# Kernel tuning notes

Measured on AMD Instinct MI355X. Metric: run time of the kernel, lower is better.

## Reference

```python
import math
import jax, jax.numpy as jnp
import numpy as np

L, H = 4, 8  # num_layers, num_heads
SPARSE_FACTOR = 0.1
NEG = -1e9


def _ln(x, g, b, eps=1e-5):
    m = jnp.mean(x, axis=-1, keepdims=True)
    v = jnp.mean(jnp.square(x - m), axis=-1, keepdims=True)
    return (x - m) * jax.lax.rsqrt(v + eps) * g + b


def _pos_enc(S, D):
    # sinusoidal PE, shape (S, 1, D) matching pe.unsqueeze(0).transpose(0,1)[:S]
    pos = np.arange(S, dtype=np.float32)[:, None]
    div = np.exp(np.arange(0, D, 2, dtype=np.float32) * (-math.log(10000.0) / D))
    pe = np.zeros((S, D), dtype=np.float32)
    pe[:, 0::2] = np.sin(pos * div)
    pe[:, 1::2] = np.cos(pos * div)
    return jnp.asarray(pe)[:, None, :]


def setup_inputs() -> dict:
    key = jax.random.key(0)
    B, S, I, D, F = 128, 512, 64, 512, 2048
    ks = jax.random.split(key, 10)
    w = lambda k, shape: jax.random.normal(k, shape, jnp.float32) * 0.02
    return {
        'x': jax.random.normal(ks[0], (B, S, I), jnp.float32),
        'W_in': w(ks[1], (I, D)), 'b_in': jnp.zeros((D,), jnp.float32),
        'ln1_g': jnp.ones((L, D), jnp.float32), 'ln1_b': jnp.zeros((L, D), jnp.float32),
        'Wq': w(ks[2], (L, D, D)), 'Wk': w(ks[3], (L, D, D)), 'Wv': w(ks[4], (L, D, D)),
        'Wo': w(ks[5], (L, D, D)), 'bo': jnp.zeros((L, D), jnp.float32),
        'ln2_g': jnp.ones((L, D), jnp.float32), 'ln2_b': jnp.zeros((L, D), jnp.float32),
        'W1': w(ks[6], (L, D, F)), 'b1': jnp.zeros((L, F), jnp.float32),
        'W2': w(ks[7], (L, F, D)), 'b2': jnp.zeros((L, D), jnp.float32),
        'lnf_g': jnp.ones((D,), jnp.float32), 'lnf_b': jnp.zeros((D,), jnp.float32),
    }


def reference(x, W_in, b_in, ln1_g, ln1_b, Wq, Wk, Wv, Wo, bo,
              ln2_g, ln2_b, W1, b1, W2, b2, lnf_g, lnf_b):
    B, S, _ = x.shape
    D = W_in.shape[1]
    dk = D // H
    # source: scores last dim == batch (view+transpose quirk); k = max(1, int(B*0.1))
    topk = max(1, int(B * SPARSE_FACTOR))
    h = jnp.swapaxes(x, 0, 1) @ W_in + b_in          # (S,B,D)
    h = h * math.sqrt(D) + _pos_enc(S, D)

    def heads(z, w):
        return jnp.swapaxes((z @ w).reshape(S, B, H, dk), 1, 2)  # (S,H,B,dk)

    def body(h, p):
        g1, bb1, wq, wk, wv, wo, bo_, g2, bb2, w1, b1_, w2, b2_ = p
        y = _ln(h, g1, bb1)
        q, k, v = heads(y, wq), heads(y, wk), heads(y, wv)
        scores = jnp.einsum('shbd,shcd->shbc', q, k) / math.sqrt(dk)  # (S,H,B,B)
        kth = jax.lax.top_k(scores, topk)[0][..., -1:]
        scores = jnp.where(scores >= kth, scores, NEG)  # top-k sparsification
        attn = jax.nn.softmax(scores, axis=-1)
        ctx = jnp.einsum('shbc,shcd->shbd', attn, v)
        ctx = jnp.swapaxes(ctx, 1, 2).reshape(S, B, D)
        h = ctx @ wo + bo_ + h                       # attn out + residual
        f = jax.nn.gelu(_ln(h, g2, bb2) @ w1 + b1_, approximate=False) @ w2 + b2_
        return h + f, None

    h, _ = jax.lax.scan(body, h, (ln1_g, ln1_b, Wq, Wk, Wv, Wo, bo,
                                  ln2_g, ln2_b, W1, b1, W2, b2))
    h = _ln(h, lnf_g, lnf_b)
    return jnp.swapaxes(h, 0, 1)                     # (B,S,D)
```

## Files before the change

### kernel.cpp

```cpp
#include <hip/hip_runtime.h>
#include <math.h>

#define S_ 512
#define B_ 128
#define D_ 512
#define I_ 64
#define F_ 2048
#define H_ 8
#define DK_ 64
#define L_ 4
#define SB_ (S_*B_)

typedef unsigned short u16;
typedef unsigned int u32;
typedef __attribute__((ext_vector_type(4))) unsigned int u32x4;
typedef __attribute__((ext_vector_type(4))) float f32x4;

__device__ __forceinline__ u16 f2bf(float f){
  u32 x = __builtin_bit_cast(u32, f);
  x += 0x7fffu + ((x >> 16) & 1u);
  return (u16)(x >> 16);
}

__device__ __forceinline__ void mfma16(f32x4& c, const u32x4& a, const u32x4& b){
  asm volatile("v_mfma_f32_16x16x32_bf16 %0, %1, %2, %0" : "+v"(c) : "v"(a), "v"(b));
}

__device__ __forceinline__ void gload16(const u16* g, u16* l){
  __builtin_amdgcn_global_load_lds((const __attribute__((address_space(1))) unsigned int*)g,
                                   (__attribute__((address_space(3))) unsigned int*)l, 16, 0, 0);
}

__device__ __forceinline__ float gelu_fast(float x){
  float u = 0.7978845608028654f * fmaf(0.044715f*x*x, x, x);
  float ae = __expf(-2.f*fabsf(u));
  float th = (1.f - ae) / (1.f + ae);
  th = (u < 0.f) ? -th : th;
  return 0.5f * x * (1.f + th);
}

__global__ void pe_kernel(float* __restrict__ pe){
  int s = blockIdx.x, d = threadIdx.x;
  float e = expf((float)(d & ~1) * (-9.210340371976184f / (float)D_));
  float arg = (float)s * e;
  pe[s*D_ + d] = (d & 1) ? cosf(arg) : sinf(arg);
}

__global__ void transpose_bf16(const float* __restrict__ src, u16* __restrict__ dst,
                               int R, int C, size_t zstride){
  __shared__ float t[32][33];
  size_t sbase = (size_t)blockIdx.z * R * C;
  size_t dbase = (size_t)blockIdx.z * zstride;
  int r0 = blockIdx.y*32, c0 = blockIdx.x*32;
  int tx = threadIdx.x, ty = threadIdx.y;
  #pragma unroll
  for (int j=0;j<4;j++)
    t[ty+j*8][tx] = src[sbase + (size_t)(r0+ty+j*8)*C + c0+tx];
  __syncthreads();
  #pragma unroll
  for (int j=0;j<4;j++)
    dst[dbase + (size_t)(c0+ty+j*8)*R + r0+tx] = f2bf(t[tx][ty+j*8]);
}

__global__ __launch_bounds__(512) void inproj_kernel(const float* __restrict__ x,
    const float* __restrict__ Win, const float* __restrict__ bin,
    const float* __restrict__ pe, float* __restrict__ h){
  __shared__ float xs[8][64];
  int t = threadIdx.x;
  float w[64];
  #pragma unroll
  for (int i=0;i<64;i++) w[i] = Win[i*D_ + t];
  float bd = bin[t];
  int r0 = blockIdx.x * 128;
  for (int batch=0; batch<16; batch++){
    int rb = r0 + batch*8;
    {
      int rr = t >> 6, i = t & 63;
      int r = rb + rr;
      int s = r >> 7, b = r & 127;
      xs[rr][i] = x[((size_t)b*S_ + s)*I_ + i];
    }
    __syncthreads();
    float acc[8];
    #pragma unroll
    for (int rr=0;rr<8;rr++) acc[rr] = 0.f;
    #pragma unroll
    for (int i4=0;i4<16;i4++){
      f32x4 xv[8];
      #pragma unroll
      for (int rr=0;rr<8;rr++) xv[rr] = *(const f32x4*)&xs[rr][i4*4];
      #pragma unroll
      for (int rr=0;rr<8;rr++){
        acc[rr] = fmaf(xv[rr][0], w[i4*4+0], acc[rr]);
        acc[rr] = fmaf(xv[rr][1], w[i4*4+1], acc[rr]);
        acc[rr] = fmaf(xv[rr][2], w[i4*4+2], acc[rr]);
        acc[rr] = fmaf(xv[rr][3], w[i4*4+3], acc[rr]);
      }
    }
    #pragma unroll
    for (int rr=0;rr<8;rr++){
      int r = rb + rr;
      int s = r >> 7;
      h[(size_t)r*D_ + t] = (acc[rr] + bd) * 22.627416997969522f + pe[s*D_ + t];
    }
    __syncthreads();
  }
}

template<int FINAL>
__global__ __launch_bounds__(256) void ln_kernel(const float* __restrict__ hsrc,
    const float* __restrict__ g, const float* __restrict__ bb,
    u16* __restrict__ outb, float* __restrict__ outf){
  int row = blockIdx.x*4 + (threadIdx.x>>6);
  int lane = threadIdx.x & 63;
  const float* hr = hsrc + (size_t)row*D_ + lane*8;
  f32x4 a0 = *(const f32x4*)hr;
  f32x4 a1 = *(const f32x4*)(hr+4);
  float v[8];
  #pragma unroll
  for (int j=0;j<4;j++){ v[j]=a0[j]; v[4+j]=a1[j]; }
  float sum = 0.f;
  #pragma unroll
  for (int j=0;j<8;j++) sum += v[j];
  #pragma unroll
  for (int m=1;m<64;m<<=1) sum += __shfl_xor(sum, m);
  float mean = sum * (1.f/(float)D_);
  float s2 = 0.f;
  #pragma unroll
  for (int j=0;j<8;j++){ float dd = v[j]-mean; s2 = fmaf(dd,dd,s2); }
  #pragma unroll
  for (int m=1;m<64;m<<=1) s2 += __shfl_xor(s2, m);
  float inv = rsqrtf(s2*(1.f/(float)D_) + 1e-5f);
  f32x4 g0 = *(const f32x4*)&g[lane*8];
  f32x4 g1 = *(const f32x4*)&g[lane*8+4];
  f32x4 b0 = *(const f32x4*)&bb[lane*8];
  f32x4 b1 = *(const f32x4*)&bb[lane*8+4];
  float o[8];
  #pragma unroll
  for (int j=0;j<4;j++){
    o[j]   = (v[j]-mean)*inv*g0[j] + b0[j];
    o[4+j] = (v[4+j]-mean)*inv*g1[j] + b1[j];
  }
  if (FINAL == 0){
    u32x4 pk;
    #pragma unroll
    for (int j=0;j<4;j++)
      pk[j] = (u32)f2bf(o[2*j]) | ((u32)f2bf(o[2*j+1])<<16);
    *(u32x4*)&outb[(size_t)row*D_ + lane*8] = pk;
  } else {
    int s = row>>7, b = row&(B_-1);
    float* op = outf + ((size_t)b*S_ + s)*D_ + lane*8;
    f32x4 r0, r1;
    #pragma unroll
    for (int j=0;j<4;j++){ r0[j]=o[j]; r1[j]=o[4+j]; }
    *(f32x4*)op = r0;
    *(f32x4*)(op+4) = r1;
  }
}

template<int MODE>
__global__ __launch_bounds__(512) void gemm256n(const u16* __restrict__ A,
    const u16* __restrict__ Wt, const float* __restrict__ bias,
    float* __restrict__ hres, u16* __restrict__ outb, int N, int K){
  const u32 nwg = gridDim.x * gridDim.y;
  u32 wg = blockIdx.y * gridDim.x + blockIdx.x;
  wg = (wg & 7) * (nwg >> 3) + (wg >> 3);
  const int m0 = (int)(wg / gridDim.x) * 128;
  const int n0 = (int)(wg % gridDim.x) * 256;
  __shared__ u16 a_lds[128*64];
  __shared__ u16 b_lds[256*64];
  const int t = threadIdx.x;
  const int lane = t & 63, wave = t >> 6;
  const int wm = wave >> 2, wn = wave & 3;
  const int rsel = lane & 15;
  const int kp0 = (((lane>>4)    ) ^ (rsel&7)) * 8;
  const int kp1 = (((lane>>4) | 4) ^ (rsel&7)) * 8;
  const int sl = (t&7) ^ ((t>>3)&7);
  const u16* ag = A  + (size_t)(m0 + (t>>3))*K + sl*8;
  const u16* bg = Wt + (size_t)(n0 + (t>>3))*K + sl*8;
  f32x4 acc[4][4] = {};
  for (int k0 = 0; k0 < K; k0 += 64){
    asm volatile("s_nop 7\n\ts_nop 7");
    __syncthreads();
    #pragma unroll
    for (int p=0;p<2;p++)
      gload16(ag + (size_t)(p*64)*K + k0, &a_lds[p*4096 + t*8]);
    #pragma unroll
    for (int p=0;p<4;p++)
      gload16(bg + (size_t)(p*64)*K + k0, &b_lds[p*4096 + t*8]);
    __syncthreads();
    u32x4 af[4], bfr[4];
    #pragma unroll
    for (int i=0;i<4;i++){
      af[i]  = *(const u32x4*)&a_lds[(wm*64 + i*16 + rsel)*64 + kp0];
      bfr[i] = *(const u32x4*)&b_lds[(wn*64 + i*16 + rsel)*64 + kp0];
    }
    #pragma unroll
    for (int i=0;i<4;i++)
      #pragma unroll
      for (int j=0;j<4;j++)
        mfma16(acc[i][j], af[i], bfr[j]);
    #pragma unroll
    for (int i=0;i<4;i++){
      af[i]  = *(const u32x4*)&a_lds[(wm*64 + i*16 + rsel)*64 + kp1];
      bfr[i] = *(const u32x4*)&b_lds[(wn*64 + i*16 + rsel)*64 + kp1];
    }
    #pragma unroll
    for (int i=0;i<4;i++)
      #pragma unroll
      for (int j=0;j<4;j++)
        mfma16(acc[i][j], af[i], bfr[j]);
  }
  asm volatile("s_nop 7\n\ts_nop 7");
  const int rb = (lane>>4)*4;
  #pragma unroll
  for (int i=0;i<4;i++){
    #pragma unroll
    for (int j=0;j<4;j++){
      int gn = n0 + wn*64 + j*16 + rsel;
      #pragma unroll
      for (int rg=0;rg<4;rg++){
        int gr = m0 + wm*64 + i*16 + rb + rg;
        float val = acc[i][j][rg];
        if (MODE == 0){
          int mat = gn >> 9;
          int hh = (gn >> 6) & 7, dd = gn & 63;
          int s = gr >> 7, b = gr & 127;
          u16* dst = outb + (size_t)mat*33554432ull;
          dst[(size_t)((s*H_ + hh)*B_ + b)*DK_ + dd] = f2bf(val);
        } else if (MODE == 1){
          hres[(size_t)gr*D_ + gn] += val + bias[gn];
        } else {
          outb[(size_t)gr*(size_t)N + gn] = f2bf(gelu_fast(val + bias[gn]));
        }
      }
    }
  }
}

template<int MODE>
__global__ __launch_bounds__(256) void gemm4w(const u16* __restrict__ A,
    const u16* __restrict__ Wt, const float* __restrict__ bias,
    float* __restrict__ hres, u16* __restrict__ outb, int N, int K){
  const u32 nwg = gridDim.x * gridDim.y;
  u32 wg = blockIdx.y * gridDim.x + blockIdx.x;
  wg = (wg & 7) * (nwg >> 3) + (wg >> 3);
  const int m0 = (int)(wg / gridDim.x) * 128;
  const int n0 = (int)(wg % gridDim.x) * 128;
  __shared__ u16 a_lds[128*32];
  __shared__ u16 b_lds[128*32];
  const int t = threadIdx.x;
  const int lane = t & 63, wave = t >> 6;
  const int wm = wave >> 1, wn = wave & 1;
  const int rsel = lane & 15;
  const int kswz = (((lane>>4) ^ ((rsel>>1)&3)) * 8);
  const int sslot = (t&3) ^ ((t>>3)&3);
  const u16* ag = A  + (size_t)(m0 + (t>>2))*K + sslot*8;
  const u16* bg = Wt + (size_t)(n0 + (t>>2))*K + sslot*8;
  f32x4 acc[4][4] = {};
  for (int k0 = 0; k0 < K; k0 += 32){
    asm volatile("s_nop 7\n\ts_nop 7");
    __syncthreads();
    gload16(ag + k0,                &a_lds[t*8]);
    gload16(ag + 64*(size_t)K + k0, &a_lds[2048 + t*8]);
    gload16(bg + k0,                &b_lds[t*8]);
    gload16(bg + 64*(size_t)K + k0, &b_lds[2048 + t*8]);
    __syncthreads();
    u32x4 af[4], bfr[4];
    #pragma unroll
    for (int i=0;i<4;i++){
      af[i]  = *(const u32x4*)&a_lds[(wm*64 + i*16 + rsel)*32 + kswz];
      bfr[i] = *(const u32x4*)&b_lds[(wn*64 + i*16 + rsel)*32 + kswz];
    }
    #pragma unroll
    for (int i=0;i<4;i++)
      #pragma unroll
      for (int j=0;j<4;j++)
        mfma16(acc[i][j], af[i], bfr[j]);
  }
  asm volatile("s_nop 7\n\ts_nop 7");
  const int rb = (lane>>4)*4;
  #pragma unroll
  for (int i=0;i<4;i++){
    #pragma unroll
    for (int j=0;j<4;j++){
      int gn = n0 + wn*64 + j*16 + rsel;
      #pragma unroll
      for (int rg=0;rg<4;rg++){
        int gr = m0 + wm*64 + i*16 + rb + rg;
        float val = acc[i][j][rg];
        if (MODE == 0){
          int mat = gn >> 9;
          int hh = (gn >> 6) & 7, dd = gn & 63;
          int s = gr >> 7, b = gr & 127;
          u16* dst = outb + (size_t)mat*33554432ull;
          dst[(size_t)((s*H_ + hh)*B_ + b)*DK_ + dd] = f2bf(val);
        } else if (MODE == 1){
          hres[(size_t)gr*D_ + gn] += val + bias[gn];
        } else {
          outb[(size_t)gr*(size_t)N + gn] = f2bf(gelu_fast(val + bias[gn]));
        }
      }
    }
  }
}

__global__ __launch_bounds__(256, 2) void attn_kernel(const u16* __restrict__ qb,
    const u16* __restrict__ kb, const u16* __restrict__ vb, u16* __restrict__ cb){
  __shared__ __align__(16) char smem[80384];
  u16* q_lds = (u16*)smem;
  u16* k_lds = (u16*)(smem + 18432);
  float* S   = (float*)smem;
  u16* P     = (u16*)smem;
  u16* vT    = (u16*)(smem + 34816);
  u32* wl    = (u32*)(smem + 67584);
  float* rs  = (float*)(smem + 79872);
  int sh = blockIdx.x;
  int s = sh >> 3, hh = sh & 7;
  int t = threadIdx.x, lane = t & 63, wave = t >> 6;
  const u16* qg = qb + (size_t)sh * (B_*DK_);
  const u16* kg = kb + (size_t)sh * (B_*DK_);
  const u16* vg = vb + (size_t)sh * (B_*DK_);
  u32x4 vr0 = *(const u32x4*)&vg[t*32];
  u32x4 vr1 = *(const u32x4*)&vg[t*32 + 8];
  u32x4 vr2 = *(const u32x4*)&vg[t*32 + 16];
  u32x4 vr3 = *(const u32x4*)&vg[t*32 + 24];
  #pragma unroll
  for (int rr=0; rr<4; rr++){
    int idx = rr*2048 + t*8;
    int row = idx >> 6, col = idx & 63;
    *(u32x4*)&q_lds[row*72+col] = *(const u32x4*)&qg[idx];
    *(u32x4*)&k_lds[row*72+col] = *(const u32x4*)&kg[idx];
  }
  __syncthreads();
  int wm = wave>>1, wn = wave&1, rsel = lane & 15;
  f32x4 sacc[4][4] = {};
  #pragma unroll
  for (int ks=0; ks<2; ks++){
    asm volatile("s_nop 7\n\ts_nop 7");
    int ko = ks*32 + (lane>>4)*8;
    u32x4 qf[4], kf[4];
    #pragma unroll
    for (int i=0;i<4;i++){
      qf[i] = *(const u32x4*)&q_lds[(wm*64+i*16+rsel)*72 + ko];
      kf[i] = *(const u32x4*)&k_lds[(wn*64+i*16+rsel)*72 + ko];
    }
    #pragma unroll
    for (int i=0;i<4;i++)
      #pragma unroll
      for (int j=0;j<4;j++)
        mfma16(sacc[i][j], qf[i], kf[j]);
  }
  asm volatile("s_nop 7\n\ts_nop 7");
  __syncthreads();
  int rb = (lane>>4)*4;
  #pragma unroll
  for (int i=0;i<4;i++)
    #pragma unroll
    for (int j=0;j<4;j++)
      #pragma unroll
      for (int rg=0;rg<4;rg++)
        S[(wm*64+i*16+rb+rg)*132 + wn*64+j*16+rsel] = sacc[i][j][rg] * 0.125f;
  __syncthreads();
  int r = t >> 1, half = t & 1;
  const f32x4* srow4 = (const f32x4*)(S + r*132 + half*64);
  float kv[12];
  #pragma unroll
  for (int i=0;i<12;i++) kv[i] = -3.4e38f;
  for (int i4=0;i4<16;i4++){
    f32x4 v4 = srow4[i4];
    float m4 = fmaxf(fmaxf(v4[0],v4[1]), fmaxf(v4[2],v4[3]));
    if (m4 > kv[11]){
      #pragma unroll
      for (int z=0; z<4; z++){
        float inc = v4[z];
        if (inc > kv[11]){
          #pragma unroll
          for (int p=0;p<12;p++){
            float cur = kv[p];
            bool gt = inc > cur;
            kv[p] = gt ? inc : cur;
            inc   = gt ? cur : inc;
          }
        }
      }
    }
  }
  float kth = 3.4e38f;
  #pragma unroll
  for (int i=0;i<12;i++){
    float pb = __shfl_xor(kv[11-i], 1);
    kth = fminf(kth, fmaxf(kv[i], pb));
  }
  float mx = fmaxf(kv[0], __shfl_xor(kv[0], 1));
  float sum = 0.f;
  int n = 0;
  u32* myw = wl + t*12;
  for (int i4=0;i4<16;i4++){
    f32x4 v4 = srow4[i4];
    #pragma unroll
    for (int z=0; z<4; z++){
      float v = v4[z];
      if (v >= kth && n < 12){
        float e = __expf(v - mx);
        sum += e;
        myw[n] = ((u32)f2bf(e) << 16) | (u32)(half*64 + i4*4 + z);
        n++;
      }
    }
  }
  float tsum = sum + __shfl_xor(sum, 1);
  if (!half) rs[r] = 1.f / tsum;
  __syncthreads();
  {
    u32x4 zz = {0u,0u,0u,0u};
    u16* pz = P + r*136 + half*64;
    #pragma unroll
    for (int z=0; z<8; z++) ((u32x4*)pz)[z] = zz;
  }
  u16* prow = P + r*136;
  for (int j=0; j<n; j++){
    u32 e = myw[j];
    prow[e & 0xffffu] = (u16)(e >> 16);
  }
  #pragma unroll
  for (int q4=0; q4<4; q4++){
    u32 u0 = (q4==0?vr0[0]:q4==1?vr1[0]:q4==2?vr2[0]:vr3[0]);
    u32 u1 = (q4==0?vr0[1]:q4==1?vr1[1]:q4==2?vr2[1]:vr3[1]);
    u32 u2 = (q4==0?vr0[2]:q4==1?vr1[2]:q4==2?vr2[2]:vr3[2]);
    u32 u3 = (q4==0?vr0[3]:q4==1?vr1[3]:q4==2?vr2[3]:vr3[3]);
    u32 uu[4] = {u0,u1,u2,u3};
    #pragma unroll
    for (int z=0; z<4; z++){
      int idx2 = t*32 + q4*8 + z*2;
      int c = idx2 >> 6, d0 = idx2 & 63;
      vT[d0*136 + c]     = (u16)(uu[z] & 0xffffu);
      vT[(d0+1)*136 + c] = (u16)(uu[z] >> 16);
    }
  }
  __syncthreads();
  f32x4 cacc[4][2] = {};
  #pragma unroll
  for (int ks=0; ks<4; ks++){
    asm volatile("s_nop 7\n\ts_nop 7");
    int ko = ks*32 + (lane>>4)*8;
    u32x4 pf[4], vf[2];
    #pragma unroll
    for (int i=0;i<4;i++) pf[i] = *(const u32x4*)&P[(wm*64+i*16+rsel)*136 + ko];
    #pragma unroll
    for (int j=0;j<2;j++) vf[j] = *(const u32x4*)&vT[(wn*32+j*16+rsel)*136 + ko];
    #pragma unroll
    for (int i=0;i<4;i++)
      #pragma unroll
      for (int j=0;j<2;j++)
        mfma16(cacc[i][j], pf[i], vf[j]);
  }
  asm volatile("s_nop 7\n\ts_nop 7");
  #pragma unroll
  for (int i=0;i<4;i++)
    #pragma unroll
    for (int j=0;j<2;j++)
      #pragma unroll
      for (int rg=0;rg<4;rg++){
        int m = wm*64 + i*16 + rb + rg;
        int nn = wn*32 + j*16 + rsel;
        float val = cacc[i][j][rg] * rs[m];
        cb[((size_t)(s*B_ + m))*D_ + hh*DK_ + nn] = f2bf(val);
      }
}

extern "C" void kernel_launch(void* const* d_in, const int* in_sizes, int n_in,
                              void* d_out, int out_size, void* d_ws, size_t ws_size,
                              hipStream_t stream) {
  const float* x    = (const float*)d_in[0];
  const float* Win  = (const float*)d_in[1];
  const float* bin  = (const float*)d_in[2];
  const float* ln1g = (const float*)d_in[3];
  const float* ln1b = (const float*)d_in[4];
  const float* Wq   = (const float*)d_in[5];
  const float* Wk   = (const float*)d_in[6];
  const float* Wv   = (const float*)d_in[7];
  const float* Wo   = (const float*)d_in[8];
  const float* bo   = (const float*)d_in[9];
  const float* ln2g = (const float*)d_in[10];
  const float* ln2b = (const float*)d_in[11];
  const float* W1   = (const float*)d_in[12];
  const float* b1   = (const float*)d_in[13];
  const float* W2   = (const float*)d_in[14];
  const float* b2   = (const float*)d_in[15];
  const float* lnfg = (const float*)d_in[16];
  const float* lnfb = (const float*)d_in[17];

  char* ws = (char*)d_ws;
  float* h  = (float*)(ws);
  u16* yb   = (u16*)(ws + 134217728ull);
  u16* qb   = (u16*)(ws + 201326592ull);
  u16* kb   = (u16*)(ws + 268435456ull);
  u16* vb   = (u16*)(ws + 335544320ull);
  u16* cb   = (u16*)(ws + 402653184ull);
  u16* act  = qb;
  u16* wqkvT= (u16*)(ws + 469762048ull);
  u16* woT  = (u16*)(ws + 476053504ull);
  u16* w1T  = (u16*)(ws + 478150656ull);
  u16* w2T  = (u16*)(ws + 486539264ull);
  float* pe = (float*)(ws + 494927872ull);

  dim3 tb(32,8);
  pe_kernel<<<S_, D_, 0, stream>>>(pe);
  transpose_bf16<<<dim3(D_/32, D_/32, L_), tb, 0, stream>>>(Wq, wqkvT,            D_, D_, (size_t)3*D_*D_);
  transpose_bf16<<<dim3(D_/32, D_/32, L_), tb, 0, stream>>>(Wk, wqkvT + D_*D_,    D_, D_, (size_t)3*D_*D_);
  transpose_bf16<<<dim3(D_/32, D_/32, L_), tb, 0, stream>>>(Wv, wqkvT + 2*D_*D_,  D_, D_, (size_t)3*D_*D_);
  transpose_bf16<<<dim3(D_/32, D_/32, L_), tb, 0, stream>>>(Wo, woT,              D_, D_, (size_t)D_*D_);
  transpose_bf16<<<dim3(F_/32, D_/32, L_), tb, 0, stream>>>(W1, w1T, D_, F_, (size_t)D_*F_);
  transpose_bf16<<<dim3(D_/32, F_/32, L_), tb, 0, stream>>>(W2, w2T, F_, D_, (size_t)F_*D_);
  inproj_kernel<<<512, 512, 0, stream>>>(x, Win, bin, pe, h);

  ln_kernel<0><<<SB_/4, 256, 0, stream>>>(h, ln1g, ln1b, yb, nullptr);
  for (int l=0; l<L_; l++){
    gemm256n<0><<<dim3(6,512), 512, 0, stream>>>(yb, wqkvT + (size_t)l*3*D_*D_, nullptr, nullptr, qb, 1536, D_);
    attn_kernel<<<S_*H_, 256, 0, stream>>>(qb, kb, vb, cb);
    gemm256n<1><<<dim3(2,512), 512, 0, stream>>>(cb, woT + (size_t)l*D_*D_, bo + l*D_, h, nullptr, D_, D_);
    ln_kernel<0><<<SB_/4, 256, 0, stream>>>(h, ln2g + l*D_, ln2b + l*D_, yb, nullptr);
    gemm4w<2><<<dim3(16,512), 256, 0, stream>>>(yb, w1T + (size_t)l*D_*F_, b1 + l*F_, nullptr, act, F_, D_);
    gemm256n<1><<<dim3(2,512), 512, 0, stream>>>(act, w2T + (size_t)l*F_*D_, b2 + l*D_, h, nullptr, D_, F_);
    if (l < L_-1)
      ln_kernel<0><<<SB_/4, 256, 0, stream>>>(h, ln1g + (l+1)*D_, ln1b + (l+1)*D_, yb, nullptr);
  }
  ln_kernel<1><<<SB_/4, 256, 0, stream>>>(h, lnfg, lnfb, nullptr, (float*)d_out);
}
```

Measured before the change: 3.429 ms.

## Double-buffer LDS tiles in both GEMM kernels to overlap global loads with MFMA

Both GEMM kernels now keep two LDS buffers. The loads for the next K tile are issued before the MFMAs on the current tile, so there is one barrier per iteration instead of two. The 256-wide kernel also drops from a 64-deep K tile to a 32-deep one with a different swizzle, which keeps the double-buffered LDS footprint the same. The aim is to hide global-to-LDS latency behind compute, at the cost of more iterations and more barriers per unit of K in the larger kernel.

```diff
diff --git a/kernel.cpp b/kernel.cpp
--- a/kernel.cpp
+++ b/kernel.cpp
@@ -167,49 +167,41 @@
   wg = (wg & 7) * (nwg >> 3) + (wg >> 3);
   const int m0 = (int)(wg / gridDim.x) * 128;
   const int n0 = (int)(wg % gridDim.x) * 256;
-  __shared__ u16 a_lds[128*64];
-  __shared__ u16 b_lds[256*64];
+  __shared__ u16 a_lds[2][128*32];
+  __shared__ u16 b_lds[2][256*32];
   const int t = threadIdx.x;
   const int lane = t & 63, wave = t >> 6;
   const int wm = wave >> 2, wn = wave & 3;
   const int rsel = lane & 15;
-  const int kp0 = (((lane>>4)    ) ^ (rsel&7)) * 8;
-  const int kp1 = (((lane>>4) | 4) ^ (rsel&7)) * 8;
-  const int sl = (t&7) ^ ((t>>3)&7);
-  const u16* ag = A  + (size_t)(m0 + (t>>3))*K + sl*8;
-  const u16* bg = Wt + (size_t)(n0 + (t>>3))*K + sl*8;
+  const int kswz = (((lane>>4) ^ ((rsel>>1)&3)) * 8);
+  const int sslot = (t&3) ^ ((t>>3)&3);
+  const u16* ag = A  + (size_t)(m0 + (t>>2))*K + sslot*8;
+  const u16* bg = Wt + (size_t)(n0 + (t>>2))*K + sslot*8;
+  const int NT = K >> 5;
+  auto stage = [&](int bsel, int kt){
+    gload16(ag + kt*32,                  &a_lds[bsel][t*8]);
+    gload16(bg + kt*32,                  &b_lds[bsel][t*8]);
+    gload16(bg + 128*(size_t)K + kt*32,  &b_lds[bsel][4096 + t*8]);
+  };
   f32x4 acc[4][4] = {};
-  for (int k0 = 0; k0 < K; k0 += 64){
+  stage(0, 0);
+  __syncthreads();
+  for (int kt = 0; kt < NT; ++kt){
+    const int cur = kt & 1;
+    if (kt + 1 < NT) stage(cur ^ 1, kt + 1);
+    u32x4 af[4], bfr[4];
+    #pragma unroll
+    for (int i=0;i<4;i++){
+      af[i]  = *(const u32x4*)&a_lds[cur][(wm*64 + i*16 + rsel)*32 + kswz];
+      bfr[i] = *(const u32x4*)&b_lds[cur][(wn*64 + i*16 + rsel)*32 + kswz];
+    }
+    #pragma unroll
+    for (int i=0;i<4;i++)
+      #pragma unroll
+      for (int j=0;j<4;j++)
+        mfma16(acc[i][j], af[i], bfr[j]);
     asm volatile("s_nop 7\n\ts_nop 7");
     __syncthreads();
-    #pragma unroll
-    for (int p=0;p<2;p++)
-      gload16(ag + (size_t)(p*64)*K + k0, &a_lds[p*4096 + t*8]);
-    #pragma unroll
-    for (int p=0;p<4;p++)
-      gload16(bg + (size_t)(p*64)*K + k0, &b_lds[p*4096 + t*8]);
-    __syncthreads();
-    u32x4 af[4], bfr[4];
-    #pragma unroll
-    for (int i=0;i<4;i++){
-      af[i]  = *(const u32x4*)&a_lds[(wm*64 + i*16 + rsel)*64 + kp0];
-      bfr[i] = *(const u32x4*)&b_lds[(wn*64 + i*16 + rsel)*64 + kp0];
-    }
-    #pragma unroll
-    for (int i=0;i<4;i++)
-      #pragma unroll
-      for (int j=0;j<4;j++)
-        mfma16(acc[i][j], af[i], bfr[j]);
-    #pragma unroll
-    for (int i=0;i<4;i++){
-      af[i]  = *(const u32x4*)&a_lds[(wm*64 + i*16 + rsel)*64 + kp1];
-      bfr[i] = *(const u32x4*)&b_lds[(wn*64 + i*16 + rsel)*64 + kp1];
-    }
-    #pragma unroll
-    for (int i=0;i<4;i++)
-      #pragma unroll
-      for (int j=0;j<4;j++)
-        mfma16(acc[i][j], af[i], bfr[j]);
   }
   asm volatile("s_nop 7\n\ts_nop 7");
   const int rb = (lane>>4)*4;
@@ -247,8 +239,8 @@
   wg = (wg & 7) * (nwg >> 3) + (wg >> 3);
   const int m0 = (int)(wg / gridDim.x) * 128;
   const int n0 = (int)(wg % gridDim.x) * 128;
-  __shared__ u16 a_lds[128*32];
-  __shared__ u16 b_lds[128*32];
+  __shared__ u16 a_lds[2][128*32];
+  __shared__ u16 b_lds[2][128*32];
   const int t = threadIdx.x;
   const int lane = t & 63, wave = t >> 6;
   const int wm = wave >> 1, wn = wave & 1;
@@ -257,26 +249,32 @@
   const int sslot = (t&3) ^ ((t>>3)&3);
   const u16* ag = A  + (size_t)(m0 + (t>>2))*K + sslot*8;
   const u16* bg = Wt + (size_t)(n0 + (t>>2))*K + sslot*8;
+  const int NT = K >> 5;
+  auto stage = [&](int bsel, int kt){
+    gload16(ag + kt*32,                 &a_lds[bsel][t*8]);
+    gload16(ag + 64*(size_t)K + kt*32,  &a_lds[bsel][2048 + t*8]);
+    gload16(bg + kt*32,                 &b_lds[bsel][t*8]);
+    gload16(bg + 64*(size_t)K + kt*32,  &b_lds[bsel][2048 + t*8]);
+  };
   f32x4 acc[4][4] = {};
-  for (int k0 = 0; k0 < K; k0 += 32){
+  stage(0, 0);
+  __syncthreads();
+  for (int kt = 0; kt < NT; ++kt){
+    const int cur = kt & 1;
+    if (kt + 1 < NT) stage(cur ^ 1, kt + 1);
+    u32x4 af[4], bfr[4];
+    #pragma unroll
+    for (int i=0;i<4;i++){
+      af[i]  = *(const u32x4*)&a_lds[cur][(wm*64 + i*16 + rsel)*32 + kswz];
+      bfr[i] = *(const u32x4*)&b_lds[cur][(wn*64 + i*16 + rsel)*32 + kswz];
+    }
+    #pragma unroll
+    for (int i=0;i<4;i++)
+      #pragma unroll
+      for (int j=0;j<4;j++)
+        mfma16(acc[i][j], af[i], bfr[j]);
     asm volatile("s_nop 7\n\ts_nop 7");
     __syncthreads();
-    gload16(ag + k0,                &a_lds[t*8]);
-    gload16(ag + 64*(size_t)K + k0, &a_lds[2048 + t*8]);
-    gload16(bg + k0,                &b_lds[t*8]);
-    gload16(bg + 64*(size_t)K + k0, &b_lds[2048 + t*8]);
-    __syncthreads();
-    u32x4 af[4], bfr[4];
-    #pragma unroll
-    for (int i=0;i<4;i++){
-      af[i]  = *(const u32x4*)&a_lds[(wm*64 + i*16 + rsel)*32 + kswz];
-      bfr[i] = *(const u32x4*)&b_lds[(wn*64 + i*16 + rsel)*32 + kswz];
-    }
-    #pragma unroll
-    for (int i=0;i<4;i++)
-      #pragma unroll
-      for (int j=0;j<4;j++)
-        mfma16(acc[i][j], af[i], bfr[j]);
   }
   asm volatile("s_nop 7\n\ts_nop 7");
   const int rb = (lane>>4)*4;
```

After: 3.553 ms. 1.04x slower.
